# Kernel tuning notes

Hardware: AMD Instinct MI355X
Metric: run time of the kernel (lower is better)

The kernel has to match this reference:

```python
import jax, jax.numpy as jnp
import numpy as np

EPS = 1e-5
GROUPS = 8


def _bn(x, gamma, beta, mean, var, axis):
    # inference-mode batchnorm along `axis`
    shape = [1] * x.ndim
    shape[axis] = -1
    scale = gamma.reshape(shape) * jax.lax.rsqrt(var.reshape(shape) + EPS)
    return (x - mean.reshape(shape)) * scale + beta.reshape(shape)


def setup_inputs() -> dict:
    key = jax.random.key(0)
    ks = jax.random.split(key, 16)
    N, C, H, W = 8, 128, 128, 128
    out_planes = 128
    x = jax.random.normal(ks[0], (N, C, H, W), jnp.float32)
    w_qkv = jax.random.normal(ks[1], (2 * out_planes, C), jnp.float32) * np.float32(np.sqrt(1.0 / C))

    def bn_params(k, c):
        k1, k2, k3, k4 = jax.random.split(k, 4)
        gamma = jax.random.uniform(k1, (c,), jnp.float32, 0.5, 1.5)
        beta = jax.random.normal(k2, (c,), jnp.float32) * 0.1
        mean = jax.random.normal(k3, (c,), jnp.float32) * 0.1
        var = jax.random.uniform(k4, (c,), jnp.float32, 0.5, 1.5)
        return gamma, beta, mean, var

    qg, qb, qm, qv = bn_params(ks[2], 2 * out_planes)
    sg, sb, sm, sv = bn_params(ks[3], GROUPS)
    og, ob, om, ov = bn_params(ks[4], out_planes)
    return {
        'x': x, 'w_qkv': w_qkv,
        'qkv_gamma': qg, 'qkv_beta': qb, 'qkv_mean': qm, 'qkv_var': qv,
        'sim_gamma': sg, 'sim_beta': sb, 'sim_mean': sm, 'sim_var': sv,
        'out_gamma': og, 'out_beta': ob, 'out_mean': om, 'out_var': ov,
    }


def reference(x, w_qkv, qkv_gamma, qkv_beta, qkv_mean, qkv_var,
              sim_gamma, sim_beta, sim_mean, sim_var,
              out_gamma, out_beta, out_mean, out_var):
    N, C, H, W = x.shape
    groups = GROUPS
    out_planes = w_qkv.shape[0] // 2
    gp = out_planes // groups  # group_planes

    # width=False: (N,C,H,W) -> (N,W,C,H) -> (N*W, C, H)
    xb = jnp.transpose(x, (0, 3, 1, 2)).reshape(N * W, C, H)
    # conv1x1 qkv transform + BN1d over channels
    qkv = jnp.einsum('bci,oc->boi', xb, w_qkv)
    qkv = _bn(qkv, qkv_gamma, qkv_beta, qkv_mean, qkv_var, axis=1)
    qkv = qkv.reshape(N * W, groups, 2 * gp, H)
    q = qkv[:, :, : gp // 2]          # (NW, g, gp/2, H)
    k = qkv[:, :, gp // 2: gp]        # (NW, g, gp/2, H)
    v = qkv[:, :, gp:]                # (NW, g, gp,   H)

    qk = jnp.einsum('bgci,bgcj->bgij', q, k)  # (NW, g, H, H)
    sim = _bn(qk, sim_gamma, sim_beta, sim_mean, sim_var, axis=1)
    sim = jax.nn.softmax(sim, axis=3)

    sv = jnp.einsum('bgij,bgcj->bgci', sim, v)  # (NW, g, gp, H)
    sv = sv.reshape(N * W, out_planes, H)
    out = _bn(sv, out_gamma, out_beta, out_mean, out_var, axis=1)
    out = out.reshape(N, W, out_planes, H)
    # permute(0,2,3,1): (N, out_planes, H, W)
    return jnp.transpose(out, (0, 2, 3, 1))
```

## Files before the change

kernel.cpp:

```cpp
#include <hip/hip_runtime.h>
#include <math.h>

#define EPS 1e-5f

typedef _Float16 half4 __attribute__((ext_vector_type(4)));
typedef _Float16 half8 __attribute__((ext_vector_type(8)));
typedef float floatx4 __attribute__((ext_vector_type(4)));

__global__ void transpose_cvt_k(const float* __restrict__ x, _Float16* __restrict__ xt2) {
  __shared__ float tile[64][65];
  int nh = blockIdx.x;
  int n = nh >> 7, h = nh & 127;
  int c0 = blockIdx.y * 64, w0 = blockIdx.z * 64;
  const float* src = x + (size_t)n * 2097152 + (size_t)h * 128;
  _Float16* dst = xt2 + (size_t)n * 2097152 + (size_t)h * 128;
  int lane = threadIdx.x & 63;
  int tr = threadIdx.x >> 6;
#pragma unroll
  for (int rr = tr; rr < 64; rr += 4)
    tile[rr][lane] = src[(size_t)(c0 + rr) * 16384 + w0 + lane];
  __syncthreads();
#pragma unroll
  for (int cc = tr; cc < 64; cc += 4)
    dst[(size_t)(w0 + cc) * 16384 + c0 + lane] = (_Float16)tile[lane][cc];
}

__global__ void __launch_bounds__(64, 2) fused_qkv_attn(
    const _Float16* __restrict__ xt2, const float* __restrict__ wq,
    const float* __restrict__ qg, const float* __restrict__ qb,
    const float* __restrict__ qm, const float* __restrict__ qv,
    const float* __restrict__ sg, const float* __restrict__ sb,
    const float* __restrict__ sm, const float* __restrict__ svv,
    const float* __restrict__ og, const float* __restrict__ ob,
    const float* __restrict__ om, const float* __restrict__ ov,
    _Float16* __restrict__ svout) {
  __shared__ _Float16 qkvlds[128 * 72];
  __shared__ _Float16 plds[16 * 136];
  int bq = blockIdx.x;
  int b = bq & 1023;
  int qtr = bq >> 10;
  int t = threadIdx.x;
  int n = t & 15;
  int q4 = t >> 4;

  const _Float16* xb = xt2 + (size_t)b * 16384;

  floatx4 acc[4][8];
#pragma unroll
  for (int mt = 0; mt < 4; mt++)
#pragma unroll
    for (int nt = 0; nt < 8; nt++)
#pragma unroll
      for (int r = 0; r < 4; r++) acc[mt][nt][r] = 0.f;

#pragma unroll
  for (int k0 = 0; k0 < 128; k0 += 32) {
    half8 af[4];
#pragma unroll
    for (int mt = 0; mt < 4; mt++) {
      const float* wp = wq + (size_t)(qtr * 64 + mt * 16 + n) * 128 + k0 + q4 * 8;
      float4 a0 = *(const float4*)wp;
      float4 a1 = *(const float4*)(wp + 4);
      half8 h;
      h[0] = (_Float16)a0.x; h[1] = (_Float16)a0.y; h[2] = (_Float16)a0.z; h[3] = (_Float16)a0.w;
      h[4] = (_Float16)a1.x; h[5] = (_Float16)a1.y; h[6] = (_Float16)a1.z; h[7] = (_Float16)a1.w;
      af[mt] = h;
    }
    half8 bf[8];
#pragma unroll
    for (int nt = 0; nt < 8; nt++)
      bf[nt] = *(const half8*)(xb + (size_t)(nt * 16 + n) * 128 + k0 + q4 * 8);
#pragma unroll
    for (int mt = 0; mt < 4; mt++)
#pragma unroll
      for (int nt = 0; nt < 8; nt++)
        acc[mt][nt] = __builtin_amdgcn_mfma_f32_16x16x32_f16(af[mt], bf[nt], acc[mt][nt], 0, 0, 0);
  }

  float qsc[4][4], qbi[4][4];
#pragma unroll
  for (int mt = 0; mt < 4; mt++)
#pragma unroll
    for (int r = 0; r < 4; r++) {
      int o = qtr * 64 + mt * 16 + q4 * 4 + r;
      float sc = qg[o] * rsqrtf(qv[o] + EPS);
      qsc[mt][r] = sc;
      qbi[mt][r] = qb[o] - qm[o] * sc;
    }

#pragma unroll
  for (int mt = 0; mt < 4; mt++)
#pragma unroll
    for (int nt = 0; nt < 8; nt++) {
      int h = nt * 16 + n;
      half4 hh;
#pragma unroll
      for (int r = 0; r < 4; r++)
        hh[r] = (_Float16)fmaf(acc[mt][nt][r], qsc[mt][r], qbi[mt][r]);
      *(half4*)(&qkvlds[h * 72 + mt * 16 + q4 * 4]) = hh;
    }

#pragma unroll 1
  for (int gl = 0; gl < 2; gl++) {
    int g = qtr * 2 + gl;
    int chb = gl * 32;

    half8 kf[8];
#pragma unroll
    for (int jt = 0; jt < 8; jt++)
      kf[jt] = *(const half8*)(&qkvlds[(jt * 16 + n) * 72 + chb + 8]);

    half8 vf[4];
#pragma unroll
    for (int ks = 0; ks < 4; ks++)
#pragma unroll
      for (int jj = 0; jj < 8; jj++)
        vf[ks][jj] = qkvlds[(ks * 32 + q4 * 8 + jj) * 72 + chb + 16 + n];

    float s_scale = sg[g] * rsqrtf(svv[g] + EPS);
    float sc4 = s_scale * 0.25f;
    float s_bias = sb[g] - sm[g] * s_scale;

    float osc[4], obi[4];
#pragma unroll
    for (int r = 0; r < 4; r++) {
      int oc = g * 16 + q4 * 4 + r;
      float s0 = og[oc] * rsqrtf(ov[oc] + EPS);
      osc[r] = s0;
      obi[r] = ob[oc] - om[oc] * s0;
    }

    for (int st8 = 0; st8 < 8; st8++) {
      half8 qf = *(const half8*)(&qkvlds[(st8 * 16 + n) * 72 + chb]);

      floatx4 stt[8];
#pragma unroll
      for (int jt = 0; jt < 8; jt++) {
        floatx4 z = {0.f, 0.f, 0.f, 0.f};
        stt[jt] = __builtin_amdgcn_mfma_f32_16x16x32_f16(kf[jt], qf, z, 0, 0, 0);
      }

      float mx = -1e30f;
#pragma unroll
      for (int jt = 0; jt < 8; jt++)
#pragma unroll
        for (int r = 0; r < 4; r++) {
          stt[jt][r] = fmaf(stt[jt][r], sc4, s_bias);
          mx = fmaxf(mx, stt[jt][r]);
        }
      mx = fmaxf(mx, __shfl_xor(mx, 16));
      mx = fmaxf(mx, __shfl_xor(mx, 32));

      float ls = 0.f;
#pragma unroll
      for (int jt = 0; jt < 8; jt++)
#pragma unroll
        for (int r = 0; r < 4; r++) {
          float e = __expf(stt[jt][r] - mx);
          stt[jt][r] = e;
          ls += e;
        }
      ls += __shfl_xor(ls, 16);
      ls += __shfl_xor(ls, 32);

#pragma unroll
      for (int jt = 0; jt < 8; jt++) {
        half4 h;
        h[0] = (_Float16)stt[jt][0];
        h[1] = (_Float16)stt[jt][1];
        h[2] = (_Float16)stt[jt][2];
        h[3] = (_Float16)stt[jt][3];
        *(half4*)(&plds[n * 136 + jt * 16 + q4 * 4]) = h;
      }

      floatx4 oacc = {0.f, 0.f, 0.f, 0.f};
#pragma unroll
      for (int ks = 0; ks < 4; ks++) {
        half8 pf = *(const half8*)(&plds[n * 136 + ks * 32 + q4 * 8]);
        oacc = __builtin_amdgcn_mfma_f32_16x16x32_f16(vf[ks], pf, oacc, 0, 0, 0);
      }

      float invl = 1.f / ls;
      _Float16* outp = svout + ((size_t)b * 128 + g * 16 + q4 * 4) * 128 + st8 * 16 + n;
#pragma unroll
      for (int r = 0; r < 4; r++)
        outp[(size_t)r * 128] = (_Float16)fmaf(oacc[r] * invl, osc[r], obi[r]);
    }
  }
}

__global__ void transpose_h2f_k(const _Float16* __restrict__ in, float* __restrict__ out,
                                int R, int C) {
  __shared__ float tile[64][65];
  int nblk = blockIdx.x;
  int r0 = blockIdx.y * 64;
  int c0 = blockIdx.z * 64;
  const _Float16* src = in + (size_t)nblk * R * C;
  float* dst = out + (size_t)nblk * R * C;
  int lane = threadIdx.x & 63;
  int tr = threadIdx.x >> 6;
#pragma unroll
  for (int rr = tr; rr < 64; rr += 4)
    tile[rr][lane] = (float)src[(size_t)(r0 + rr) * C + c0 + lane];
  __syncthreads();
#pragma unroll
  for (int cc = tr; cc < 64; cc += 4)
    dst[(size_t)(c0 + cc) * R + r0 + lane] = tile[lane][cc];
}

extern "C" void kernel_launch(void* const* d_in, const int* in_sizes, int n_in,
                              void* d_out, int out_size, void* d_ws, size_t ws_size,
                              hipStream_t stream) {
  const float* x  = (const float*)d_in[0];
  const float* wq = (const float*)d_in[1];
  const float* qg = (const float*)d_in[2];
  const float* qb = (const float*)d_in[3];
  const float* qm = (const float*)d_in[4];
  const float* qv = (const float*)d_in[5];
  const float* sg = (const float*)d_in[6];
  const float* sb = (const float*)d_in[7];
  const float* sm = (const float*)d_in[8];
  const float* sv = (const float*)d_in[9];
  const float* og = (const float*)d_in[10];
  const float* ob = (const float*)d_in[11];
  const float* om = (const float*)d_in[12];
  const float* ov = (const float*)d_in[13];
  float* out = (float*)d_out;

  _Float16* xt2 = (_Float16*)d_ws;
  _Float16* svh = xt2 + (size_t)1024 * 128 * 128;

  transpose_cvt_k<<<dim3(1024, 2, 2), 256, 0, stream>>>(x, xt2);
  fused_qkv_attn<<<4096, 64, 0, stream>>>(xt2, wq, qg, qb, qm, qv,
                                          sg, sb, sm, sv, og, ob, om, ov, svh);
  transpose_h2f_k<<<dim3(8, 2, 256), 256, 0, stream>>>(svh, out, 128, 16384);
}
```

Before: 265.1 us.

## Split fused QKV-attention kernel into separate QKV GEMM and attention kernels

After: 285.6 us. +7.8%, slower.

```diff
diff --git a/kernel.cpp b/kernel.cpp
--- a/kernel.cpp
+++ b/kernel.cpp
@@ -25,40 +25,46 @@
     dst[(size_t)(w0 + cc) * 16384 + c0 + lane] = (_Float16)tile[lane][cc];
 }
 
-__global__ void __launch_bounds__(64, 2) fused_qkv_attn(
+__global__ void qkv_mfma2(
     const _Float16* __restrict__ xt2, const float* __restrict__ wq,
     const float* __restrict__ qg, const float* __restrict__ qb,
     const float* __restrict__ qm, const float* __restrict__ qv,
-    const float* __restrict__ sg, const float* __restrict__ sb,
-    const float* __restrict__ sm, const float* __restrict__ svv,
-    const float* __restrict__ og, const float* __restrict__ ob,
-    const float* __restrict__ om, const float* __restrict__ ov,
-    _Float16* __restrict__ svout) {
-  __shared__ _Float16 qkvlds[128 * 72];
-  __shared__ _Float16 plds[16 * 136];
-  int bq = blockIdx.x;
-  int b = bq & 1023;
-  int qtr = bq >> 10;
+    _Float16* __restrict__ qkv2) {
+  __shared__ _Float16 Bs[64 * 136];
+  int blk = blockIdx.x;
+  int b = blk >> 1, ih = blk & 1;
   int t = threadIdx.x;
-  int n = t & 15;
-  int q4 = t >> 4;
-
-  const _Float16* xb = xt2 + (size_t)b * 16384;
-
-  floatx4 acc[4][8];
+
+  const _Float16* xb = xt2 + (size_t)b * 16384 + (size_t)ih * 64 * 128;
+#pragma unroll
+  for (int idx = t; idx < 1024; idx += 256) {
+    int row = idx >> 4, cg = idx & 15;
+    int cgs = cg ^ ((row & 1) << 2);
+    *(half8*)(&Bs[row * 136 + cgs * 8]) = *(const half8*)(xb + (size_t)row * 128 + cg * 8);
+  }
+  __syncthreads();
+
+  int wv = t >> 6;
+  int lane = t & 63;
+  int n = lane & 15;
+  int q4 = lane >> 4;
+  int ob = wv * 64;
+
+  floatx4 acc[4][4];
 #pragma unroll
   for (int mt = 0; mt < 4; mt++)
 #pragma unroll
-    for (int nt = 0; nt < 8; nt++)
+    for (int nt = 0; nt < 4; nt++)
 #pragma unroll
       for (int r = 0; r < 4; r++) acc[mt][nt][r] = 0.f;
 
 #pragma unroll
-  for (int k0 = 0; k0 < 128; k0 += 32) {
+  for (int ks = 0; ks < 4; ks++) {
+    int k0 = ks * 32;
     half8 af[4];
 #pragma unroll
     for (int mt = 0; mt < 4; mt++) {
-      const float* wp = wq + (size_t)(qtr * 64 + mt * 16 + n) * 128 + k0 + q4 * 8;
+      const float* wp = wq + (size_t)(ob + mt * 16 + n) * 128 + k0 + q4 * 8;
       float4 a0 = *(const float4*)wp;
       float4 a1 = *(const float4*)(wp + 4);
       half8 h;
@@ -66,14 +72,17 @@
       h[4] = (_Float16)a1.x; h[5] = (_Float16)a1.y; h[6] = (_Float16)a1.z; h[7] = (_Float16)a1.w;
       af[mt] = h;
     }
-    half8 bf[8];
-#pragma unroll
-    for (int nt = 0; nt < 8; nt++)
-      bf[nt] = *(const half8*)(xb + (size_t)(nt * 16 + n) * 128 + k0 + q4 * 8);
+    half8 bf[4];
+#pragma unroll
+    for (int nt = 0; nt < 4; nt++) {
+      int row = nt * 16 + n;
+      int cg = (ks * 4 + q4) ^ ((row & 1) << 2);
+      bf[nt] = *(const half8*)(&Bs[row * 136 + cg * 8]);
+    }
 #pragma unroll
     for (int mt = 0; mt < 4; mt++)
 #pragma unroll
-      for (int nt = 0; nt < 8; nt++)
+      for (int nt = 0; nt < 4; nt++)
         acc[mt][nt] = __builtin_amdgcn_mfma_f32_16x16x32_f16(af[mt], bf[nt], acc[mt][nt], 0, 0, 0);
   }
 
@@ -82,110 +91,125 @@
   for (int mt = 0; mt < 4; mt++)
 #pragma unroll
     for (int r = 0; r < 4; r++) {
-      int o = qtr * 64 + mt * 16 + q4 * 4 + r;
+      int o = ob + mt * 16 + q4 * 4 + r;
       float sc = qg[o] * rsqrtf(qv[o] + EPS);
       qsc[mt][r] = sc;
       qbi[mt][r] = qb[o] - qm[o] * sc;
     }
 
+  _Float16* outb = qkv2 + (size_t)b * 32768;
 #pragma unroll
   for (int mt = 0; mt < 4; mt++)
 #pragma unroll
-    for (int nt = 0; nt < 8; nt++) {
-      int h = nt * 16 + n;
+    for (int nt = 0; nt < 4; nt++) {
+      int i = ih * 64 + nt * 16 + n;
       half4 hh;
 #pragma unroll
       for (int r = 0; r < 4; r++)
         hh[r] = (_Float16)fmaf(acc[mt][nt][r], qsc[mt][r], qbi[mt][r]);
-      *(half4*)(&qkvlds[h * 72 + mt * 16 + q4 * 4]) = hh;
-    }
-
-#pragma unroll 1
-  for (int gl = 0; gl < 2; gl++) {
-    int g = qtr * 2 + gl;
-    int chb = gl * 32;
-
-    half8 kf[8];
+      *(half4*)(outb + (size_t)i * 256 + ob + mt * 16 + q4 * 4) = hh;
+    }
+}
+
+__global__ void __launch_bounds__(64) attn_mfma_kernel(
+    const _Float16* __restrict__ qkv2,
+    const float* __restrict__ sg, const float* __restrict__ sb,
+    const float* __restrict__ sm, const float* __restrict__ svv,
+    const float* __restrict__ og, const float* __restrict__ ob,
+    const float* __restrict__ om, const float* __restrict__ ov,
+    _Float16* __restrict__ svout) {
+  __shared__ _Float16 plds[16 * 136];
+  int bg = blockIdx.x;
+  int b = bg >> 3, g = bg & 7;
+  int t = threadIdx.x;
+  int n = t & 15;
+  int q4 = t >> 4;
+
+  const _Float16* base = qkv2 + (size_t)b * 32768 + g * 32;
+
+  half8 kf[8];
+#pragma unroll
+  for (int jt = 0; jt < 8; jt++)
+    kf[jt] = *(const half8*)(base + (size_t)(jt * 16 + n) * 256 + 8);
+
+  half8 vf[4];
+#pragma unroll
+  for (int ks = 0; ks < 4; ks++)
+#pragma unroll
+    for (int jj = 0; jj < 8; jj++)
+      vf[ks][jj] = base[(size_t)(ks * 32 + q4 * 8 + jj) * 256 + 16 + n];
+
+  float s_scale = sg[g] * rsqrtf(svv[g] + EPS);
+  float sc4 = s_scale * 0.25f;
+  float s_bias = sb[g] - sm[g] * s_scale;
+
+  float osc[4], obi[4];
+#pragma unroll
+  for (int r = 0; r < 4; r++) {
+    int oc = g * 16 + q4 * 4 + r;
+    float s0 = og[oc] * rsqrtf(ov[oc] + EPS);
+    osc[r] = s0;
+    obi[r] = ob[oc] - om[oc] * s0;
+  }
+
+  for (int st8 = 0; st8 < 8; st8++) {
+    half8 qf = *(const half8*)(base + (size_t)(st8 * 16 + n) * 256);
+
+    floatx4 stt[8];
+#pragma unroll
+    for (int jt = 0; jt < 8; jt++) {
+      floatx4 z = {0.f, 0.f, 0.f, 0.f};
+      stt[jt] = __builtin_amdgcn_mfma_f32_16x16x32_f16(kf[jt], qf, z, 0, 0, 0);
+    }
+
+    float mx = -1e30f;
 #pragma unroll
     for (int jt = 0; jt < 8; jt++)
-      kf[jt] = *(const half8*)(&qkvlds[(jt * 16 + n) * 72 + chb + 8]);
-
-    half8 vf[4];
-#pragma unroll
-    for (int ks = 0; ks < 4; ks++)
-#pragma unroll
-      for (int jj = 0; jj < 8; jj++)
-        vf[ks][jj] = qkvlds[(ks * 32 + q4 * 8 + jj) * 72 + chb + 16 + n];
-
-    float s_scale = sg[g] * rsqrtf(svv[g] + EPS);
-    float sc4 = s_scale * 0.25f;
-    float s_bias = sb[g] - sm[g] * s_scale;
-
-    float osc[4], obi[4];
-#pragma unroll
-    for (int r = 0; r < 4; r++) {
-      int oc = g * 16 + q4 * 4 + r;
-      float s0 = og[oc] * rsqrtf(ov[oc] + EPS);
-      osc[r] = s0;
-      obi[r] = ob[oc] - om[oc] * s0;
-    }
-
-    for (int st8 = 0; st8 < 8; st8++) {
-      half8 qf = *(const half8*)(&qkvlds[(st8 * 16 + n) * 72 + chb]);
-
-      floatx4 stt[8];
-#pragma unroll
-      for (int jt = 0; jt < 8; jt++) {
-        floatx4 z = {0.f, 0.f, 0.f, 0.f};
-        stt[jt] = __builtin_amdgcn_mfma_f32_16x16x32_f16(kf[jt], qf, z, 0, 0, 0);
+#pragma unroll
+      for (int r = 0; r < 4; r++) {
+        stt[jt][r] = fmaf(stt[jt][r], sc4, s_bias);
+        mx = fmaxf(mx, stt[jt][r]);
       }
-
-      float mx = -1e30f;
-#pragma unroll
-      for (int jt = 0; jt < 8; jt++)
-#pragma unroll
-        for (int r = 0; r < 4; r++) {
-          stt[jt][r] = fmaf(stt[jt][r], sc4, s_bias);
-          mx = fmaxf(mx, stt[jt][r]);
-        }
-      mx = fmaxf(mx, __shfl_xor(mx, 16));
-      mx = fmaxf(mx, __shfl_xor(mx, 32));
-
-      float ls = 0.f;
-#pragma unroll
-      for (int jt = 0; jt < 8; jt++)
-#pragma unroll
-        for (int r = 0; r < 4; r++) {
-          float e = __expf(stt[jt][r] - mx);
-          stt[jt][r] = e;
-          ls += e;
-        }
-      ls += __shfl_xor(ls, 16);
-      ls += __shfl_xor(ls, 32);
-
-#pragma unroll
-      for (int jt = 0; jt < 8; jt++) {
-        half4 h;
-        h[0] = (_Float16)stt[jt][0];
-        h[1] = (_Float16)stt[jt][1];
-        h[2] = (_Float16)stt[jt][2];
-        h[3] = (_Float16)stt[jt][3];
-        *(half4*)(&plds[n * 136 + jt * 16 + q4 * 4]) = h;
+    mx = fmaxf(mx, __shfl_xor(mx, 16));
+    mx = fmaxf(mx, __shfl_xor(mx, 32));
+
+    float ls = 0.f;
+#pragma unroll
+    for (int jt = 0; jt < 8; jt++)
+#pragma unroll
+      for (int r = 0; r < 4; r++) {
+        float e = __expf(stt[jt][r] - mx);
+        stt[jt][r] = e;
+        ls += e;
       }
-
-      floatx4 oacc = {0.f, 0.f, 0.f, 0.f};
-#pragma unroll
-      for (int ks = 0; ks < 4; ks++) {
-        half8 pf = *(const half8*)(&plds[n * 136 + ks * 32 + q4 * 8]);
-        oacc = __builtin_amdgcn_mfma_f32_16x16x32_f16(vf[ks], pf, oacc, 0, 0, 0);
-      }
-
-      float invl = 1.f / ls;
-      _Float16* outp = svout + ((size_t)b * 128 + g * 16 + q4 * 4) * 128 + st8 * 16 + n;
-#pragma unroll
-      for (int r = 0; r < 4; r++)
-        outp[(size_t)r * 128] = (_Float16)fmaf(oacc[r] * invl, osc[r], obi[r]);
-    }
+    ls += __shfl_xor(ls, 16);
+    ls += __shfl_xor(ls, 32);
+
+#pragma unroll
+    for (int jt = 0; jt < 8; jt++) {
+      half4 h;
+      h[0] = (_Float16)stt[jt][0];
+      h[1] = (_Float16)stt[jt][1];
+      h[2] = (_Float16)stt[jt][2];
+      h[3] = (_Float16)stt[jt][3];
+      int jg8 = jt * 2 + (q4 >> 1);
+      int off = n * 136 + (jg8 ^ ((n & 1) << 2)) * 8 + (q4 & 1) * 4;
+      *(half4*)(&plds[off]) = h;
+    }
+
+    floatx4 oacc = {0.f, 0.f, 0.f, 0.f};
+#pragma unroll
+    for (int ks = 0; ks < 4; ks++) {
+      int jg8 = ks * 4 + q4;
+      half8 pf = *(const half8*)(&plds[n * 136 + (jg8 ^ ((n & 1) << 2)) * 8]);
+      oacc = __builtin_amdgcn_mfma_f32_16x16x32_f16(vf[ks], pf, oacc, 0, 0, 0);
+    }
+
+    float invl = 1.f / ls;
+    _Float16* outp = svout + ((size_t)b * 128 + g * 16 + q4 * 4) * 128 + st8 * 16 + n;
+#pragma unroll
+    for (int r = 0; r < 4; r++)
+      outp[(size_t)r * 128] = (_Float16)fmaf(oacc[r] * invl, osc[r], obi[r]);
   }
 }
 
@@ -228,10 +252,11 @@
   float* out = (float*)d_out;
 
   _Float16* xt2 = (_Float16*)d_ws;
-  _Float16* svh = xt2 + (size_t)1024 * 128 * 128;
+  _Float16* qkv2 = xt2 + (size_t)1024 * 128 * 128;
+  _Float16* svh = qkv2 + (size_t)1024 * 128 * 256;
 
   transpose_cvt_k<<<dim3(1024, 2, 2), 256, 0, stream>>>(x, xt2);
-  fused_qkv_attn<<<4096, 64, 0, stream>>>(xt2, wq, qg, qb, qm, qv,
-                                          sg, sb, sm, sv, og, ob, om, ov, svh);
+  qkv_mfma2<<<2048, 256, 0, stream>>>(xt2, wq, qg, qb, qm, qv, qkv2);
+  attn_mfma_kernel<<<8192, 64, 0, stream>>>(qkv2, sg, sb, sm, sv, og, ob, om, ov, svh);
   transpose_h2f_k<<<dim3(8, 2, 256), 256, 0, stream>>>(svh, out, 128, 16384);
 }
```
